# Optimization experiments

Hardware: AMD Instinct MI355X
Metric: run time of the kernel (lower is better)

Reference implementation:

```python
import jax, jax.numpy as jnp
import numpy as np

N_EMBD = 1024
N_HEAD = 16
HEAD_DIM = N_EMBD // N_HEAD
B, T = 2, 2048


def setup_inputs() -> dict:
    key = jax.random.key(0)
    ks = jax.random.split(key, 9)
    s = 1.0 / np.sqrt(N_EMBD)
    return {
        "x": jax.random.normal(ks[0], (B, T, N_EMBD), dtype=jnp.float32),
        "Wq": jax.random.normal(ks[1], (N_EMBD, N_EMBD), dtype=jnp.float32) * s,
        "bq": jax.random.normal(ks[2], (N_EMBD,), dtype=jnp.float32) * s,
        "Wk": jax.random.normal(ks[3], (N_EMBD, N_EMBD), dtype=jnp.float32) * s,
        "bk": jax.random.normal(ks[4], (N_EMBD,), dtype=jnp.float32) * s,
        "Wv": jax.random.normal(ks[5], (N_EMBD, N_EMBD), dtype=jnp.float32) * s,
        "bv": jax.random.normal(ks[6], (N_EMBD,), dtype=jnp.float32) * s,
        "Wp": jax.random.normal(ks[7], (N_EMBD, N_EMBD), dtype=jnp.float32) * s,
        "bp": jax.random.normal(ks[8], (N_EMBD,), dtype=jnp.float32) * s,
    }


def reference(x, Wq, bq, Wk, bk, Wv, bv, Wp, bp):
    b, t, c = x.shape
    # torch Linear: y = x @ W.T + b
    def proj(W, bias):
        y = jnp.einsum('btc,oc->bto', x, W) + bias
        return y.reshape(b, t, N_HEAD, HEAD_DIM).transpose(0, 2, 1, 3)  # [B,H,T,D]

    q = proj(Wq, bq)
    k = proj(Wk, bk)
    v = proj(Wv, bv)

    scale = 1.0 / np.sqrt(HEAD_DIM).astype(np.float32)
    scores = jnp.einsum('bhqd,bhkd->bhqk', q, k) * scale  # [B,H,T,T]
    causal = jnp.tril(jnp.ones((t, t), dtype=bool))
    scores = jnp.where(causal[None, None], scores, jnp.float32(-jnp.inf))
    attn = jax.nn.softmax(scores, axis=-1)
    out = jnp.einsum('bhqk,bhkd->bhqd', attn, v)  # [B,H,T,D]
    out = out.transpose(0, 2, 1, 3).reshape(b, t, c)
    out = jnp.einsum('btc,oc->bto', out, Wp) + bp
    return out
```

## Files before the change

### kernel.cpp

```cpp
#include <hip/hip_runtime.h>
#include <hip/hip_bf16.h>

#define TT 2048
#define MM 4096
#define KS_LD 72

typedef __attribute__((ext_vector_type(8))) short bf16x8;
typedef __attribute__((ext_vector_type(4))) float f32x4;

__device__ inline short f2bf(float f){
  union { float f; unsigned u; } x; x.f = f;
  unsigned r = x.u + 0x7FFFu + ((x.u >> 16) & 1u);
  return (short)(r >> 16);
}

__device__ inline void async16(const void* g, void* l){
  __builtin_amdgcn_global_load_lds((const __attribute__((address_space(1))) void*)g,
                                   (__attribute__((address_space(3))) void*)l, 16, 0, 0);
}

__global__ void cvt_all(const float* __restrict__ x,
                        const float* __restrict__ Wq, const float* __restrict__ Wk,
                        const float* __restrict__ Wv, const float* __restrict__ Wp,
                        short* __restrict__ xb, short* __restrict__ Wqb, short* __restrict__ Wkb,
                        short* __restrict__ Wvb, short* __restrict__ Wpb){
  int b = blockIdx.x;
  const float* in; short* out; int base;
  if (b < 4096)      { in = x;  out = xb;  base = b; }
  else if (b < 5120) { in = Wq; out = Wqb; base = b - 4096; }
  else if (b < 6144) { in = Wk; out = Wkb; base = b - 5120; }
  else if (b < 7168) { in = Wv; out = Wvb; base = b - 6144; }
  else               { in = Wp; out = Wpb; base = b - 7168; }
  int i = base * 256 + threadIdx.x;
  float4 v = ((const float4*)in)[i];
  short4 o;
  o.x = f2bf(v.x); o.y = f2bf(v.y); o.z = f2bf(v.z); o.w = f2bf(v.w);
  ((short4*)out)[i] = o;
}

__device__ inline void gemm_core(const short* __restrict__ A, const short* __restrict__ Wm,
                                 short* As, short* Bs, int m0, int n0,
                                 int tid, int wm, int wn, int quad, int lr,
                                 f32x4 acc[4][4])
{
  const int row = tid >> 2, col = (tid & 3) << 3;
  const short* Ap0 = A  + (size_t)(m0 + row) * 1024 + col;
  const short* Ap1 = A  + (size_t)(m0 + row + 64) * 1024 + col;
  const short* Bp0 = Wm + (size_t)(n0 + row) * 1024 + col;
  const short* Bp1 = Wm + (size_t)(n0 + row + 64) * 1024 + col;
  for (int kt = 0; kt < 32; ++kt){
    const int kk = kt * 32;
    async16(Ap0 + kk, As + (size_t)tid * 8);
    async16(Ap1 + kk, As + (size_t)(tid + 256) * 8);
    async16(Bp0 + kk, Bs + (size_t)tid * 8);
    async16(Bp1 + kk, Bs + (size_t)(tid + 256) * 8);
    __syncthreads();
    bf16x8 aF[4], bF[4];
#pragma unroll
    for (int mt = 0; mt < 4; ++mt) aF[mt] = *(const bf16x8*)(As + (wm*64 + mt*16 + lr)*32 + quad*8);
#pragma unroll
    for (int nt = 0; nt < 4; ++nt) bF[nt] = *(const bf16x8*)(Bs + (wn*64 + nt*16 + lr)*32 + quad*8);
#pragma unroll
    for (int mt = 0; mt < 4; ++mt)
#pragma unroll
      for (int nt = 0; nt < 4; ++nt)
        acc[mt][nt] = __builtin_amdgcn_mfma_f32_16x16x32_bf16(aF[mt], bF[nt], acc[mt][nt], 0, 0, 0);
    __syncthreads();
  }
}

__launch_bounds__(256, 3)
__global__ void gemm_qkv(const short* __restrict__ A,
                         const short* __restrict__ W0, const short* __restrict__ W1, const short* __restrict__ W2,
                         const float* __restrict__ b0, const float* __restrict__ b1, const float* __restrict__ b2,
                         short* __restrict__ Qo, short* __restrict__ Ko, short* __restrict__ Vt)
{
  __shared__ __align__(16) short smem[9216];
  short* As = smem;
  short* Bs = smem + 4096;
  const int z = blockIdx.z;
  const short* Wm   = (z == 0) ? W0 : ((z == 1) ? W1 : W2);
  const float* bias = (z == 0) ? b0 : ((z == 1) ? b1 : b2);
  const int tid = threadIdx.x;
  const int lane = tid & 63, wave = tid >> 6;
  const int wm = wave >> 1, wn = wave & 1;
  const int quad = lane >> 4, lr = lane & 15;
  const int m0 = blockIdx.y * 128, n0 = blockIdx.x * 128;

  f32x4 acc[4][4];
#pragma unroll
  for (int i = 0; i < 4; ++i)
#pragma unroll
    for (int j = 0; j < 4; ++j)
#pragma unroll
      for (int r = 0; r < 4; ++r) acc[i][j][r] = 0.f;

  gemm_core(A, Wm, As, Bs, m0, n0, tid, wm, wn, quad, lr, acc);

  const float qscale = 0.125f * 1.4426950408889634f;
  const int bB = m0 >> 11, t0 = m0 & 2047;

  if (z == 2){
#pragma unroll
    for (int nh = 0; nh < 2; ++nh){
      __syncthreads();
      if (wn == nh){
#pragma unroll
        for (int nt = 0; nt < 4; ++nt){
          int n = n0 + wn*64 + nt*16 + lr;
          float bv = bias[n];
          int n_l = nt*16 + lr;
#pragma unroll
          for (int mt = 0; mt < 4; ++mt)
#pragma unroll
            for (int r = 0; r < 4; ++r){
              int m_l = wm*64 + mt*16 + quad*4 + r;
              smem[n_l*136 + m_l] = f2bf(acc[mt][nt][r] + bv);
            }
        }
      }
      __syncthreads();
#pragma unroll
      for (int i = 0; i < 4; ++i){
        int c = tid + i*256;
        int rowN = c >> 4, ch = c & 15;
        int4 v = *(const int4*)(smem + rowN*136 + ch*8);
        int n = n0 + nh*64 + rowN;
        int hH = n >> 6, d = n & 63;
        *(int4*)(Vt + ((size_t)((bB<<4) + hH)*64 + d)*2048 + t0 + ch*8) = v;
      }
    }
    return;
  }

  short* dst = (z == 0) ? Qo : Ko;
#pragma unroll
  for (int nh = 0; nh < 2; ++nh){
    __syncthreads();
    if (wn == nh){
#pragma unroll
      for (int nt = 0; nt < 4; ++nt){
        int n_l = nt*16 + lr;
        float bv = bias[n0 + nh*64 + n_l];
#pragma unroll
        for (int mt = 0; mt < 4; ++mt){
#pragma unroll
          for (int r = 0; r < 4; ++r){
            int m_l = wm*64 + mt*16 + quad*4 + r;
            float v = acc[mt][nt][r] + bv;
            if (z == 0) v *= qscale;
            smem[m_l*72 + n_l] = f2bf(v);
          }
        }
      }
    }
    __syncthreads();
    const int hH = (n0 + nh*64) >> 6;
    short* dhead = dst + (size_t)((bB<<4) + hH) * 2048 * 64;
#pragma unroll
    for (int i = 0; i < 4; ++i){
      int c = tid + i*256;
      int rowm = c >> 3, ch = (c & 7) << 3;
      int4 v = *(const int4*)(smem + rowm*72 + ch);
      *(int4*)(dhead + (size_t)(t0 + rowm)*64 + ch) = v;
    }
  }
}

__launch_bounds__(256, 2)
__global__ void gemm_proj(const short* __restrict__ A, const short* __restrict__ Wm,
                          const float* __restrict__ bias, float* __restrict__ out)
{
  __shared__ __align__(16) short As[128*32];
  __shared__ __align__(16) short Bs[64*32];
  const int tid = threadIdx.x;
  const int lane = tid & 63, wave = tid >> 6;
  const int quad = lane >> 4, lr = lane & 15;
  const int m0 = blockIdx.y * 128, n0 = blockIdx.x * 64;

  const int row = tid >> 2, col = (tid & 3) << 3;
  const short* Ap0 = A  + (size_t)(m0 + row) * 1024 + col;
  const short* Ap1 = A  + (size_t)(m0 + row + 64) * 1024 + col;
  const short* Bp0 = Wm + (size_t)(n0 + row) * 1024 + col;

  f32x4 acc[2][4];
#pragma unroll
  for (int i = 0; i < 2; ++i)
#pragma unroll
    for (int j = 0; j < 4; ++j)
#pragma unroll
      for (int r = 0; r < 4; ++r) acc[i][j][r] = 0.f;

  for (int kt = 0; kt < 32; ++kt){
    const int kk = kt * 32;
    async16(Ap0 + kk, As + (size_t)tid * 8);
    async16(Ap1 + kk, As + (size_t)(tid + 256) * 8);
    if (row < 64) async16(Bp0 + kk, Bs + (size_t)tid * 8);
    __syncthreads();
    bf16x8 aF[2], bF[4];
#pragma unroll
    for (int mt = 0; mt < 2; ++mt) aF[mt] = *(const bf16x8*)(As + (wave*32 + mt*16 + lr)*32 + quad*8);
#pragma unroll
    for (int nt = 0; nt < 4; ++nt) bF[nt] = *(const bf16x8*)(Bs + (nt*16 + lr)*32 + quad*8);
#pragma unroll
    for (int mt = 0; mt < 2; ++mt)
#pragma unroll
      for (int nt = 0; nt < 4; ++nt)
        acc[mt][nt] = __builtin_amdgcn_mfma_f32_16x16x32_bf16(aF[mt], bF[nt], acc[mt][nt], 0, 0, 0);
    __syncthreads();
  }

#pragma unroll
  for (int nt = 0; nt < 4; ++nt){
    int n = n0 + nt*16 + lr;
    float bv = bias[n];
#pragma unroll
    for (int mt = 0; mt < 2; ++mt){
      int mBase = m0 + wave*32 + mt*16 + quad*4;
#pragma unroll
      for (int r = 0; r < 4; ++r){
        int m = mBase + r;
        out[(size_t)m * 1024 + n] = acc[mt][nt][r] + bv;
      }
    }
  }
}

__launch_bounds__(256, 4)
__global__ void attn_kernel(const short* __restrict__ Q, const short* __restrict__ K,
                            const short* __restrict__ Vt, short* __restrict__ AO)
{
  __shared__ __align__(16) short Ks[64*KS_LD];
  __shared__ __align__(16) short Vs[64*KS_LD];
  __shared__ __align__(16) short Ps[4*16*KS_LD];
  const int tid = threadIdx.x, lane = tid & 63, wave = tid >> 6;
  const int quad = lane >> 4, lr = lane & 15;
  const int bid = blockIdx.x;
  const int qt = 31 - (bid >> 5);
  const int hb = bid & 31;
  const int bidx = hb >> 4, h = hb & 15;
  const int q0 = qt * 64;
  const int wq = q0 + wave * 16;
  const short* Qh = Q  + (size_t)hb * TT * 64;
  const short* Kh = K  + (size_t)hb * TT * 64;
  const short* Vh = Vt + (size_t)hb * 64 * TT;
  short* Pw = Ps + wave * 16 * KS_LD;

  bf16x8 qf[2];
#pragma unroll
  for (int ks = 0; ks < 2; ++ks)
    qf[ks] = *(const bf16x8*)(Qh + (size_t)(wq + lr) * 64 + ks*32 + quad*8);

  f32x4 acc_o[4], l_acc;
#pragma unroll
  for (int r = 0; r < 4; ++r) l_acc[r] = 0.f;
#pragma unroll
  for (int dt = 0; dt < 4; ++dt)
#pragma unroll
    for (int r = 0; r < 4; ++r) acc_o[dt][r] = 0.f;

  const short one_bf = (short)0x3F80;
  const bf16x8 onesf = { one_bf, one_bf, one_bf, one_bf, one_bf, one_bf, one_bf, one_bf };

  const int srow = tid >> 3, scol = (tid & 7) << 3;

  const int nkv = qt + 1;
  for (int kv = 0; kv < nkv; ++kv){
    const int kv0 = kv * 64;
    __syncthreads();
#pragma unroll
    for (int s = 0; s < 2; ++s){
      *(int4*)(Ks + (srow + s*32) * KS_LD + scol) = *(const int4*)(Kh + (size_t)(kv0 + srow + s*32) * 64 + scol);
      *(int4*)(Vs + (srow + s*32) * KS_LD + scol) = *(const int4*)(Vh + (size_t)(srow + s*32) * TT + kv0 + scol);
    }
    __syncthreads();
    if (kv0 > wq + 15) continue;

    f32x4 s4[4];
#pragma unroll
    for (int nt = 0; nt < 4; ++nt)
#pragma unroll
      for (int r = 0; r < 4; ++r) s4[nt][r] = 0.f;
#pragma unroll
    for (int nt = 0; nt < 4; ++nt)
#pragma unroll
      for (int ks = 0; ks < 2; ++ks){
        bf16x8 kf = *(const bf16x8*)(Ks + (nt*16 + lr)*KS_LD + ks*32 + quad*8);
        s4[nt] = __builtin_amdgcn_mfma_f32_16x16x32_bf16(qf[ks], kf, s4[nt], 0, 0, 0);
      }

    const bool need_mask = (kv == nkv - 1);
    const int prow = quad * 4;
    const int qg = wq + prow;
#pragma unroll
    for (int nt = 0; nt < 4; ++nt){
      const int key = kv0 + nt*16 + lr;
      float pv[4];
#pragma unroll
      for (int r = 0; r < 4; ++r){
        float v = exp2f(s4[nt][r]);
        if (need_mask && key > qg + r) v = 0.f;
        pv[r] = v;
      }
#pragma unroll
      for (int rp = 0; rp < 2; ++rp){
        __hip_bfloat162 h2 = __float22bfloat162_rn(make_float2(pv[2*rp], pv[2*rp+1]));
        unsigned u = *(unsigned*)&h2;
        Pw[(prow + 2*rp    )*KS_LD + nt*16 + lr] = (short)(u & 0xffffu);
        Pw[(prow + 2*rp + 1)*KS_LD + nt*16 + lr] = (short)(u >> 16);
      }
    }

#pragma unroll
    for (int ks = 0; ks < 2; ++ks){
      bf16x8 pf = *(const bf16x8*)(Pw + lr*KS_LD + ks*32 + quad*8);
      l_acc = __builtin_amdgcn_mfma_f32_16x16x32_bf16(pf, onesf, l_acc, 0, 0, 0);
#pragma unroll
      for (int dt = 0; dt < 4; ++dt){
        bf16x8 vf = *(const bf16x8*)(Vs + (dt*16 + lr)*KS_LD + ks*32 + quad*8);
        acc_o[dt] = __builtin_amdgcn_mfma_f32_16x16x32_bf16(pf, vf, acc_o[dt], 0, 0, 0);
      }
    }
  }

  float inv[4];
#pragma unroll
  for (int r = 0; r < 4; ++r) inv[r] = __builtin_amdgcn_rcpf(l_acc[r]);
#pragma unroll
  for (int dt = 0; dt < 4; ++dt){
    int d = dt*16 + lr;
#pragma unroll
    for (int r = 0; r < 4; ++r){
      int qg = wq + quad*4 + r;
      AO[(size_t)(bidx*2048 + qg)*1024 + h*64 + d] = f2bf(acc_o[dt][r] * inv[r]);
    }
  }
}

extern "C" void kernel_launch(void* const* d_in, const int* in_sizes, int n_in,
                              void* d_out, int out_size, void* d_ws, size_t ws_size,
                              hipStream_t stream)
{
  const float* x  = (const float*)d_in[0];
  const float* Wq = (const float*)d_in[1];
  const float* bq = (const float*)d_in[2];
  const float* Wk = (const float*)d_in[3];
  const float* bk = (const float*)d_in[4];
  const float* Wv = (const float*)d_in[5];
  const float* bv = (const float*)d_in[6];
  const float* Wp = (const float*)d_in[7];
  const float* bp = (const float*)d_in[8];
  float* out = (float*)d_out;

  char* ws = (char*)d_ws;
  const size_t MB = 1024ull * 1024ull;
  short* Qb  = (short*)(ws + 0);
  short* Kb  = (short*)(ws + 8*MB);
  short* Vtb = (short*)(ws + 16*MB);
  short* AOb = (short*)(ws + 24*MB);
  short* xb  = (short*)(ws + 32*MB);
  short* Wqb = (short*)(ws + 40*MB);
  short* Wkb = (short*)(ws + 42*MB);
  short* Wvb = (short*)(ws + 44*MB);
  short* Wpb = (short*)(ws + 46*MB);

  cvt_all<<<8192, 256, 0, stream>>>(x, Wq, Wk, Wv, Wp, xb, Wqb, Wkb, Wvb, Wpb);
  gemm_qkv<<<dim3(8, 32, 3), 256, 0, stream>>>(xb, Wqb, Wkb, Wvb, bq, bk, bv, Qb, Kb, Vtb);
  attn_kernel<<<1024, 256, 0, stream>>>(Qb, Kb, Vtb, AOb);
  gemm_proj<<<dim3(16, 32), 256, 0, stream>>>(AOb, Wpb, bp, out);
}
```

Measured before the change: 188.9 us.

## Double K-step in GEMMs, transpose attention MFMA operands, vectorize P and output stores

```diff
diff --git a/kernel.cpp b/kernel.cpp
--- a/kernel.cpp
+++ b/kernel.cpp
@@ -12,6 +12,10 @@
   union { float f; unsigned u; } x; x.f = f;
   unsigned r = x.u + 0x7FFFu + ((x.u >> 16) & 1u);
   return (short)(r >> 16);
+}
+__device__ inline int pk2bf(float a, float b){
+  __hip_bfloat162 h2 = __float22bfloat162_rn(make_float2(a, b));
+  return *(int*)&h2;
 }
 
 __device__ inline void async16(const void* g, void* l){
@@ -43,28 +47,34 @@
                                  int tid, int wm, int wn, int quad, int lr,
                                  f32x4 acc[4][4])
 {
-  const int row = tid >> 2, col = (tid & 3) << 3;
-  const short* Ap0 = A  + (size_t)(m0 + row) * 1024 + col;
-  const short* Ap1 = A  + (size_t)(m0 + row + 64) * 1024 + col;
-  const short* Bp0 = Wm + (size_t)(n0 + row) * 1024 + col;
-  const short* Bp1 = Wm + (size_t)(n0 + row + 64) * 1024 + col;
-  for (int kt = 0; kt < 32; ++kt){
-    const int kk = kt * 32;
-    async16(Ap0 + kk, As + (size_t)tid * 8);
-    async16(Ap1 + kk, As + (size_t)(tid + 256) * 8);
-    async16(Bp0 + kk, Bs + (size_t)tid * 8);
-    async16(Bp1 + kk, Bs + (size_t)(tid + 256) * 8);
-    __syncthreads();
-    bf16x8 aF[4], bF[4];
-#pragma unroll
-    for (int mt = 0; mt < 4; ++mt) aF[mt] = *(const bf16x8*)(As + (wm*64 + mt*16 + lr)*32 + quad*8);
-#pragma unroll
-    for (int nt = 0; nt < 4; ++nt) bF[nt] = *(const bf16x8*)(Bs + (wn*64 + nt*16 + lr)*32 + quad*8);
-#pragma unroll
-    for (int mt = 0; mt < 4; ++mt)
-#pragma unroll
-      for (int nt = 0; nt < 4; ++nt)
-        acc[mt][nt] = __builtin_amdgcn_mfma_f32_16x16x32_bf16(aF[mt], bF[nt], acc[mt][nt], 0, 0, 0);
+  const int prow = tid >> 2, pcol = (tid & 3) << 3;
+  const short* Ap0 = A  + (size_t)(m0 + prow) * 1024 + pcol;
+  const short* Ap1 = A  + (size_t)(m0 + prow + 64) * 1024 + pcol;
+  const short* Bp0 = Wm + (size_t)(n0 + prow) * 1024 + pcol;
+  const short* Bp1 = Wm + (size_t)(n0 + prow + 64) * 1024 + pcol;
+  for (int kt = 0; kt < 16; ++kt){
+    const int kk = kt * 64;
+#pragma unroll
+    for (int pn = 0; pn < 2; ++pn){
+      async16(Ap0 + kk + pn*32, As + pn*4096 + (size_t)tid * 8);
+      async16(Ap1 + kk + pn*32, As + pn*4096 + (size_t)(tid + 256) * 8);
+      async16(Bp0 + kk + pn*32, Bs + pn*4096 + (size_t)tid * 8);
+      async16(Bp1 + kk + pn*32, Bs + pn*4096 + (size_t)(tid + 256) * 8);
+    }
+    __syncthreads();
+#pragma unroll
+    for (int ks = 0; ks < 2; ++ks){
+      bf16x8 aF[4], bF[4];
+#pragma unroll
+      for (int mt = 0; mt < 4; ++mt) aF[mt] = *(const bf16x8*)(As + ks*4096 + (wm*64 + mt*16 + lr)*32 + quad*8);
+#pragma unroll
+      for (int nt = 0; nt < 4; ++nt) bF[nt] = *(const bf16x8*)(Bs + ks*4096 + (wn*64 + nt*16 + lr)*32 + quad*8);
+#pragma unroll
+      for (int mt = 0; mt < 4; ++mt)
+#pragma unroll
+        for (int nt = 0; nt < 4; ++nt)
+          acc[mt][nt] = __builtin_amdgcn_mfma_f32_16x16x32_bf16(aF[mt], bF[nt], acc[mt][nt], 0, 0, 0);
+    }
     __syncthreads();
   }
 }
@@ -75,9 +85,9 @@
                          const float* __restrict__ b0, const float* __restrict__ b1, const float* __restrict__ b2,
                          short* __restrict__ Qo, short* __restrict__ Ko, short* __restrict__ Vt)
 {
-  __shared__ __align__(16) short smem[9216];
+  __shared__ __align__(16) short smem[16384];
   short* As = smem;
-  short* Bs = smem + 4096;
+  short* Bs = smem + 8192;
   const int z = blockIdx.z;
   const short* Wm   = (z == 0) ? W0 : ((z == 1) ? W1 : W2);
   const float* bias = (z == 0) ? b0 : ((z == 1) ? b1 : b2);
@@ -171,17 +181,17 @@
 __global__ void gemm_proj(const short* __restrict__ A, const short* __restrict__ Wm,
                           const float* __restrict__ bias, float* __restrict__ out)
 {
-  __shared__ __align__(16) short As[128*32];
-  __shared__ __align__(16) short Bs[64*32];
+  __shared__ __align__(16) short As[2*4096];
+  __shared__ __align__(16) short Bs[2*2048];
   const int tid = threadIdx.x;
   const int lane = tid & 63, wave = tid >> 6;
   const int quad = lane >> 4, lr = lane & 15;
   const int m0 = blockIdx.y * 128, n0 = blockIdx.x * 64;
 
-  const int row = tid >> 2, col = (tid & 3) << 3;
-  const short* Ap0 = A  + (size_t)(m0 + row) * 1024 + col;
-  const short* Ap1 = A  + (size_t)(m0 + row + 64) * 1024 + col;
-  const short* Bp0 = Wm + (size_t)(n0 + row) * 1024 + col;
+  const int prow = tid >> 2, pcol = (tid & 3) << 3;
+  const short* Ap0 = A  + (size_t)(m0 + prow) * 1024 + pcol;
+  const short* Ap1 = A  + (size_t)(m0 + prow + 64) * 1024 + pcol;
+  const short* Bp0 = Wm + (size_t)(n0 + (tid >> 2)) * 1024 + pcol;
 
   f32x4 acc[2][4];
 #pragma unroll
@@ -191,22 +201,28 @@
 #pragma unroll
       for (int r = 0; r < 4; ++r) acc[i][j][r] = 0.f;
 
-  for (int kt = 0; kt < 32; ++kt){
-    const int kk = kt * 32;
-    async16(Ap0 + kk, As + (size_t)tid * 8);
-    async16(Ap1 + kk, As + (size_t)(tid + 256) * 8);
-    if (row < 64) async16(Bp0 + kk, Bs + (size_t)tid * 8);
-    __syncthreads();
-    bf16x8 aF[2], bF[4];
-#pragma unroll
-    for (int mt = 0; mt < 2; ++mt) aF[mt] = *(const bf16x8*)(As + (wave*32 + mt*16 + lr)*32 + quad*8);
-#pragma unroll
-    for (int nt = 0; nt < 4; ++nt) bF[nt] = *(const bf16x8*)(Bs + (nt*16 + lr)*32 + quad*8);
-#pragma unroll
-    for (int mt = 0; mt < 2; ++mt)
-#pragma unroll
-      for (int nt = 0; nt < 4; ++nt)
-        acc[mt][nt] = __builtin_amdgcn_mfma_f32_16x16x32_bf16(aF[mt], bF[nt], acc[mt][nt], 0, 0, 0);
+  for (int kt = 0; kt < 16; ++kt){
+    const int kk = kt * 64;
+#pragma unroll
+    for (int pn = 0; pn < 2; ++pn){
+      async16(Ap0 + kk + pn*32, As + pn*4096 + (size_t)tid * 8);
+      async16(Ap1 + kk + pn*32, As + pn*4096 + (size_t)(tid + 256) * 8);
+      async16(Bp0 + kk + pn*32, Bs + pn*2048 + (size_t)tid * 8);
+    }
+    __syncthreads();
+#pragma unroll
+    for (int ks = 0; ks < 2; ++ks){
+      bf16x8 aF[2], bF[4];
+#pragma unroll
+      for (int mt = 0; mt < 2; ++mt) aF[mt] = *(const bf16x8*)(As + ks*4096 + (wave*32 + mt*16 + lr)*32 + quad*8);
+#pragma unroll
+      for (int nt = 0; nt < 4; ++nt) bF[nt] = *(const bf16x8*)(Bs + ks*2048 + (nt*16 + lr)*32 + quad*8);
+#pragma unroll
+      for (int mt = 0; mt < 2; ++mt)
+#pragma unroll
+        for (int nt = 0; nt < 4; ++nt)
+          acc[mt][nt] = __builtin_amdgcn_mfma_f32_16x16x32_bf16(aF[mt], bF[nt], acc[mt][nt], 0, 0, 0);
+    }
     __syncthreads();
   }
 
@@ -286,54 +302,53 @@
 #pragma unroll
       for (int ks = 0; ks < 2; ++ks){
         bf16x8 kf = *(const bf16x8*)(Ks + (nt*16 + lr)*KS_LD + ks*32 + quad*8);
-        s4[nt] = __builtin_amdgcn_mfma_f32_16x16x32_bf16(qf[ks], kf, s4[nt], 0, 0, 0);
+        s4[nt] = __builtin_amdgcn_mfma_f32_16x16x32_bf16(kf, qf[ks], s4[nt], 0, 0, 0);
       }
 
     const bool need_mask = (kv == nkv - 1);
-    const int prow = quad * 4;
-    const int qg = wq + prow;
+    const int qglob = wq + lr;
 #pragma unroll
     for (int nt = 0; nt < 4; ++nt){
-      const int key = kv0 + nt*16 + lr;
+      const int keyb = kv0 + nt*16 + quad*4;
       float pv[4];
 #pragma unroll
       for (int r = 0; r < 4; ++r){
         float v = exp2f(s4[nt][r]);
-        if (need_mask && key > qg + r) v = 0.f;
+        if (need_mask && keyb + r > qglob) v = 0.f;
         pv[r] = v;
       }
-#pragma unroll
-      for (int rp = 0; rp < 2; ++rp){
-        __hip_bfloat162 h2 = __float22bfloat162_rn(make_float2(pv[2*rp], pv[2*rp+1]));
-        unsigned u = *(unsigned*)&h2;
-        Pw[(prow + 2*rp    )*KS_LD + nt*16 + lr] = (short)(u & 0xffffu);
-        Pw[(prow + 2*rp + 1)*KS_LD + nt*16 + lr] = (short)(u >> 16);
-      }
+      int2 w;
+      w.x = pk2bf(pv[0], pv[1]);
+      w.y = pk2bf(pv[2], pv[3]);
+      *(int2*)(Pw + lr*KS_LD + nt*16 + quad*4) = w;
     }
 
 #pragma unroll
     for (int ks = 0; ks < 2; ++ks){
-      bf16x8 pf = *(const bf16x8*)(Pw + lr*KS_LD + ks*32 + quad*8);
-      l_acc = __builtin_amdgcn_mfma_f32_16x16x32_bf16(pf, onesf, l_acc, 0, 0, 0);
+      bf16x8 ptf = *(const bf16x8*)(Pw + lr*KS_LD + ks*32 + quad*8);
+      l_acc = __builtin_amdgcn_mfma_f32_16x16x32_bf16(onesf, ptf, l_acc, 0, 0, 0);
 #pragma unroll
       for (int dt = 0; dt < 4; ++dt){
         bf16x8 vf = *(const bf16x8*)(Vs + (dt*16 + lr)*KS_LD + ks*32 + quad*8);
-        acc_o[dt] = __builtin_amdgcn_mfma_f32_16x16x32_bf16(pf, vf, acc_o[dt], 0, 0, 0);
-      }
-    }
-  }
-
-  float inv[4];
-#pragma unroll
-  for (int r = 0; r < 4; ++r) inv[r] = __builtin_amdgcn_rcpf(l_acc[r]);
+        acc_o[dt] = __builtin_amdgcn_mfma_f32_16x16x32_bf16(vf, ptf, acc_o[dt], 0, 0, 0);
+      }
+    }
+  }
+
+  const float inv = __builtin_amdgcn_rcpf(l_acc[0]);
 #pragma unroll
   for (int dt = 0; dt < 4; ++dt){
-    int d = dt*16 + lr;
-#pragma unroll
-    for (int r = 0; r < 4; ++r){
-      int qg = wq + quad*4 + r;
-      AO[(size_t)(bidx*2048 + qg)*1024 + h*64 + d] = f2bf(acc_o[dt][r] * inv[r]);
-    }
+    int2 w;
+    w.x = pk2bf(acc_o[dt][0] * inv, acc_o[dt][1] * inv);
+    w.y = pk2bf(acc_o[dt][2] * inv, acc_o[dt][3] * inv);
+    *(int2*)(Pw + lr*KS_LD + dt*16 + quad*4) = w;
+  }
+#pragma unroll
+  for (int i = 0; i < 2; ++i){
+    int c = lane + i*64;
+    int row = c >> 3, ch = c & 7;
+    int4 v = *(const int4*)(Pw + row*KS_LD + ch*8);
+    *(int4*)(AO + (size_t)(bidx*2048 + wq + row)*1024 + h*64 + ch*8) = v;
   }
 }
 
@@ -358,11 +373,11 @@
   short* Kb  = (short*)(ws + 8*MB);
   short* Vtb = (short*)(ws + 16*MB);
   short* AOb = (short*)(ws + 24*MB);
-  short* xb  = (short*)(ws + 32*MB);
-  short* Wqb = (short*)(ws + 40*MB);
-  short* Wkb = (short*)(ws + 42*MB);
-  short* Wvb = (short*)(ws + 44*MB);
-  short* Wpb = (short*)(ws + 46*MB);
+  short* xb  = (short*)(ws + 24*MB);
+  short* Wqb = (short*)(ws + 32*MB);
+  short* Wkb = (short*)(ws + 34*MB);
+  short* Wvb = (short*)(ws + 36*MB);
+  short* Wpb = (short*)(ws + 38*MB);
 
   cvt_all<<<8192, 256, 0, stream>>>(x, Wq, Wk, Wv, Wp, xb, Wqb, Wkb, Wvb, Wpb);
   gemm_qkv<<<dim3(8, 32, 3), 256, 0, stream>>>(xb, Wqb, Wkb, Wvb, bq, bk, bv, Qb, Kb, Vtb);
```

Result: no change. 187.2 us (-0.9%).
